# Kernel optimization log

Measured on AMD Instinct MI355X. Metric: run time of the kernel, lower is better.

## Reference

```python
import jax, jax.numpy as jnp
import numpy as np

D_STATE = 16
D_CONV = 4


def _ln_cf(x, w, b, eps=1e-6):
    # channels_first LayerNorm over dim 1 of (B,C,H,W)
    u = x.mean(1, keepdims=True)
    s = ((x - u) ** 2).mean(1, keepdims=True)
    return w[:, None, None] * ((x - u) / jnp.sqrt(s + eps)) + b[:, None, None]


def _ln_last(x, w, b, eps=1e-5):
    u = x.mean(-1, keepdims=True)
    s = ((x - u) ** 2).mean(-1, keepdims=True)
    return (x - u) / jnp.sqrt(s + eps) * w + b


def _mamba(xn, Win, convw, convb, Wx, Wdt, bdt, Alog, Dp):
    # xn: (B, L, d_model); returns (B, L, d_inner) (out_proj is Identity in this module)
    B, L, _ = xn.shape
    di = Win.shape[0] // 2
    xz = xn @ Win.T                                   # (B,L,2*di), in_proj bias=False
    xc, z = xz[..., :di], xz[..., di:]
    # causal depthwise conv1d along L (pad left d_conv-1, slice == torch pad+trim)
    xt = jnp.pad(xc.transpose(0, 2, 1), ((0, 0), (0, 0), (D_CONV - 1, 0)))
    xt = jax.lax.conv_general_dilated(xt, convw[:, None, :], (1,), 'VALID',
                                      dimension_numbers=('NCH', 'OIH', 'NCH'),
                                      feature_group_count=di)
    xs = jax.nn.silu(xt + convb[None, :, None]).transpose(0, 2, 1)  # (B,L,di)
    dtr = Wdt.shape[1]
    x_dbl = xs @ Wx.T                                 # (B,L,dtr+2*ds)
    dt = x_dbl[..., :dtr]
    Bm = x_dbl[..., dtr:dtr + D_STATE]                # (B,L,ds)
    Cm = x_dbl[..., dtr + D_STATE:]                   # (B,L,ds)
    delta = jax.nn.softplus(dt @ Wdt.T + bdt)         # (B,L,di)
    A = -jnp.exp(Alog)                                # (di,ds)
    dA = jnp.exp(delta[..., None] * A)                # (B,L,di,ds)
    dBx = delta[..., None] * Bm[:, :, None, :] * xs[..., None]

    def step(h, ab):
        a, b2 = ab
        h = a * h + b2
        return h, h

    h0 = jnp.zeros((B, di, D_STATE), xn.dtype)
    _, hs = jax.lax.scan(step, h0, (dA.transpose(1, 0, 2, 3), dBx.transpose(1, 0, 2, 3)))
    y = jnp.einsum('lbds,bls->bld', hs, Cm) + xs * Dp
    return y * jax.nn.silu(z)


def _dwconv2d(u, k, dil):
    c = k.shape[0]
    return jax.lax.conv_general_dilated(u, k[:, None], (1, 1),
                                        [(dil, dil), (dil, dil)],
                                        rhs_dilation=(dil, dil),
                                        dimension_numbers=('NCHW', 'OIHW', 'NCHW'),
                                        feature_group_count=c)


def _block(x, gamma1, gamma2, ln1_w, ln1_b, mn_w, mn_b,
           f_Win, f_convw, f_convb, f_Wx, f_Wdt, f_bdt, f_Alog, f_D,
           b_Win, b_convw, b_convb, b_Wx, b_Wdt, b_bdt, b_Alog, b_D,
           Wout, msff_win, msff_dw1, msff_dw2, msff_dw3, msff_wout):
    B, C, H, W = x.shape
    L = H * W
    # --- BiPixelMambaLayer branch ---
    x1 = _ln_cf(x, ln1_w, ln1_b)                       # norm1 (channels_first)
    xf = x1.reshape(B, C, L).transpose(0, 2, 1)        # (B,L,C)
    xn = _ln_last(xf, mn_w, mn_b)                      # inner nn.LayerNorm (eps=1e-5)
    yf = _mamba(xn, f_Win, f_convw, f_convb, f_Wx, f_Wdt, f_bdt, f_Alog, f_D)
    yb = _mamba(xn[:, ::-1], b_Win, b_convw, b_convb, b_Wx, b_Wdt, b_bdt, b_Alog, b_D)
    yo = (yf + yb[:, ::-1]) @ Wout.T                   # shared out_proj (bias=False)
    x = x + gamma1[:, None, None] * (yo.transpose(0, 2, 1).reshape(B, C, H, W) + x1)
    # --- MSFF branch (norm1 reused) ---
    inp = x
    xm = _ln_cf(x, ln1_w, ln1_b)
    h = jnp.einsum('oc,bchw->bohw', msff_win, xm)      # project_in (1x1x1 conv, depth=1)
    hid = msff_dw1.shape[0]
    h1 = _dwconv2d(h[:, :hid], msff_dw1, 1)            # Conv3d 3x3x3 w/ depth=1 == 2D center slice
    h2 = _dwconv2d(h[:, hid:2 * hid], msff_dw2, 2)
    h3 = _dwconv2d(h[:, 2 * hid:], msff_dw3, 3)
    g = jax.nn.gelu(h1, approximate=False) * h2 * h3
    xm = jnp.einsum('oc,bchw->bohw', msff_wout, g)     # project_out
    return inp + gamma2[:, None, None] * xm


def setup_inputs() -> dict:
    key = jax.random.key(0)
    ks = jax.random.split(key, 40)
    dim, di, dtr, ds, hid, Bn, H, W = 96, 192, 6, 16, 192, 2, 64, 64
    r = lambda i, shape, s=0.05: jax.random.normal(ks[i], shape, jnp.float32) * s
    inp = {
        'x': r(0, (Bn, dim, H, W), 1.0),
        'gamma1': r(1, (dim,), 0.1), 'gamma2': r(2, (dim,), 0.1),
        'ln1_w': 1.0 + r(3, (dim,), 0.1), 'ln1_b': r(4, (dim,), 0.1),
        'mn_w': 1.0 + r(5, (dim,), 0.1), 'mn_b': r(6, (dim,), 0.1),
    }
    i = 7
    for p in ('f_', 'b_'):
        inp[p + 'Win'] = r(i, (2 * di, dim)); i += 1
        inp[p + 'convw'] = r(i, (di, D_CONV), 0.2); i += 1
        inp[p + 'convb'] = r(i, (di,), 0.1); i += 1
        inp[p + 'Wx'] = r(i, (dtr + 2 * ds, di)); i += 1
        inp[p + 'Wdt'] = r(i, (di, dtr), 0.1); i += 1
        inp[p + 'bdt'] = r(i, (di,), 0.1); i += 1
        inp[p + 'Alog'] = jax.random.uniform(ks[i], (di, ds), jnp.float32, 0.0, 2.5); i += 1
        inp[p + 'D'] = r(i, (di,), 0.5); i += 1
    inp['Wout'] = r(i, (dim, di)); i += 1
    inp['msff_win'] = r(i, (3 * hid, dim)); i += 1
    inp['msff_dw1'] = r(i, (hid, 3, 3), 0.2); i += 1
    inp['msff_dw2'] = r(i, (hid, 3, 3), 0.2); i += 1
    inp['msff_dw3'] = r(i, (hid, 3, 3), 0.2); i += 1
    inp['msff_wout'] = r(i, (dim, hid)); i += 1
    return inp


def reference(x, gamma1, gamma2, ln1_w, ln1_b, mn_w, mn_b,
              f_Win, f_convw, f_convb, f_Wx, f_Wdt, f_bdt, f_Alog, f_D,
              b_Win, b_convw, b_convb, b_Wx, b_Wdt, b_bdt, b_Alog, b_D,
              Wout, msff_win, msff_dw1, msff_dw2, msff_dw3, msff_wout):
    return _block(x, gamma1, gamma2, ln1_w, ln1_b, mn_w, mn_b,
                  f_Win, f_convw, f_convb, f_Wx, f_Wdt, f_bdt, f_Alog, f_D,
                  b_Win, b_convw, b_convb, b_Wx, b_Wdt, b_bdt, b_Alog, b_D,
                  Wout, msff_win, msff_dw1, msff_dw2, msff_dw3, msff_wout)
```

## Files before the change

kernel.cpp:

```cpp
#include <hip/hip_runtime.h>
#include <hip/hip_bf16.h>
#include <math.h>

typedef __hip_bfloat16 bf16;
typedef _Float16 f16;
typedef f16  f16x8  __attribute__((ext_vector_type(8)));
typedef short short8 __attribute__((ext_vector_type(8)));
typedef unsigned short ushort8 __attribute__((ext_vector_type(8)));
typedef float floatx4 __attribute__((ext_vector_type(4)));

#define L_SEQ 4096
#define BATCH 2
#define DIM   96
#define DI    192
#define DS    16
#define HID   192
#define NPOS  (BATCH * L_SEQ)
#define NCH   256
#define CHUNK 16
#define GRP   16
#define NGRP  (NCH / GRP)
#define NREC  (2 * BATCH * DI)
#define LDBL  40
#define PLANE (4 * NCH * DI * 8)
#define LOG2E 1.44269504088896f
#define TP    32

__device__ __forceinline__ float silu_f(float x) { return x / (1.f + __expf(-x)); }
__device__ __forceinline__ float softplus_f(float x) {
    return fmaxf(x, 0.f) + __logf(1.f + __expf(-fabsf(x)));
}
__device__ __forceinline__ float b2f(bf16 v) { return __bfloat162float(v); }
__device__ __forceinline__ float us2f(unsigned short u) {
    union { unsigned int i; float f; } cv; cv.i = ((unsigned int)u) << 16; return cv.f;
}

__global__ void k_ln12_prep(const float* __restrict__ x,
                            const float* __restrict__ ln1w, const float* __restrict__ ln1b,
                            const float* __restrict__ mnw,  const float* __restrict__ mnb,
                            bf16* __restrict__ XNbf,
                            const float* __restrict__ fWin, const float* __restrict__ bWin,
                            const float* __restrict__ fWx,  const float* __restrict__ bWx,
                            const float* __restrict__ Wout, const float* __restrict__ mwin,
                            const float* __restrict__ mwout,
                            const float* __restrict__ fAlog, const float* __restrict__ bAlog,
                            const float* __restrict__ mdw1, const float* __restrict__ mdw2,
                            const float* __restrict__ mdw3,
                            bf16* __restrict__ war, float* __restrict__ a2tab,
                            float* __restrict__ mdwt) {
    __shared__ float xt[DIM][TP + 1];
    __shared__ float rs[8][TP], rss[8][TP];
    __shared__ float uu[TP], rr[TP];
    if (blockIdx.x >= NPOS / TP) {
        int i = (blockIdx.x - NPOS / TP) * 256 + threadIdx.x;
        if (i < 180480) {
            float v;
            if (i < 36864)        v = fWin[i];
            else if (i < 73728)   v = bWin[i - 36864];
            else if (i < 81024)   v = fWx[i - 73728];
            else if (i < 88320)   v = bWx[i - 81024];
            else if (i < 106752)  v = Wout[i - 88320];
            else if (i < 162048)  v = mwin[i - 106752];
            else                  v = mwout[i - 162048];
            war[i] = __float2bfloat16(v);
        } else if (i < 186624) {
            int j = i - 180480;
            int dirq = j / 3072, rem = j % 3072;
            const float* al = dirq ? bAlog : fAlog;
            a2tab[j] = -__expf(al[rem]) * LOG2E;
        } else if (i < 191808) {
            int j = i - 186624;
            int cv = j / 1728, rem = j % 1728;
            int tap = rem / 192, c = rem % 192;
            const float* src = (cv == 0) ? mdw1 : (cv == 1) ? mdw2 : mdw3;
            mdwt[j] = src[c * 9 + tap];
        }
        return;
    }
    int p0 = blockIdx.x * TP;
    int b = p0 >> 12, l0 = p0 & (L_SEQ - 1);
    int t = threadIdx.x;
    int tg = t >> 5, li = t & 31;

    for (int idx = t; idx < DIM * TP; idx += 256) {
        int c = idx >> 5, q = idx & 31;
        xt[c][q] = x[((size_t)(b * DIM + c)) * L_SEQ + l0 + q];
    }
    __syncthreads();
    {
        float s = 0.f, ss = 0.f;
        for (int c = tg; c < DIM; c += 8) { float v = xt[c][li]; s += v; ss += v * v; }
        rs[tg][li] = s; rss[tg][li] = ss;
    }
    __syncthreads();
    if (t < TP) {
        float s = 0.f, ss = 0.f;
#pragma unroll
        for (int g = 0; g < 8; g++) { s += rs[g][t]; ss += rss[g][t]; }
        float u = s / DIM;
        uu[t] = u; rr[t] = rsqrtf(ss / DIM - u * u + 1e-6f);
    }
    __syncthreads();
    {
        float u = uu[li], r = rr[li];
        float s2 = 0.f, ss2 = 0.f;
        for (int c = tg; c < DIM; c += 8) {
            float tv = ln1w[c] * (xt[c][li] - u) * r + ln1b[c];
            xt[c][li] = tv;
            s2 += tv; ss2 += tv * tv;
        }
        rs[tg][li] = s2; rss[tg][li] = ss2;
    }
    __syncthreads();
    if (t < TP) {
        float s = 0.f, ss = 0.f;
#pragma unroll
        for (int g = 0; g < 8; g++) { s += rs[g][t]; ss += rss[g][t]; }
        float u = s / DIM;
        uu[t] = u; rr[t] = rsqrtf(ss / DIM - u * u + 1e-5f);
    }
    __syncthreads();
    for (int idx = t; idx < DIM * TP; idx += 256) {
        int q = idx / DIM, c = idx % DIM;
        XNbf[(size_t)(p0 + q) * DIM + c] =
            __float2bfloat16((xt[c][q] - uu[q]) * rr[q] * mnw[c] + mnb[c]);
    }
}

__global__ void mfma_nt_dir(const bf16* __restrict__ A0, const bf16* __restrict__ A1,
                            const bf16* __restrict__ W0, const bf16* __restrict__ W1,
                            void* __restrict__ C0, void* __restrict__ C1,
                            int M, int N, int K, int ldc, int pad6, int obf) {
    int z = blockIdx.z;
    const bf16* A = z ? A1 : A0;
    const bf16* W = z ? W1 : W0;
    void* C = z ? C1 : C0;
    int wave = threadIdx.x >> 6, lane = threadIdx.x & 63;
    int m0 = blockIdx.x * 64 + wave * 16;
    int n0 = blockIdx.y * 64;
    int lm = lane & 15, quad = lane >> 4;
    const short* Ap = (const short*)A + (size_t)(m0 + lm) * K + quad * 8;
    const short* Wp = (const short*)W;
    floatx4 acc[4];
#pragma unroll
    for (int t = 0; t < 4; t++) acc[t] = (floatx4){0.f, 0.f, 0.f, 0.f};
    for (int k0 = 0; k0 < K; k0 += 32) {
        short8 a = *(const short8*)(Ap + k0);
#pragma unroll
        for (int t = 0; t < 4; t++) {
            int n = n0 + t * 16 + lm;
            short8 b = (n < N) ? *(const short8*)(Wp + (size_t)n * K + k0 + quad * 8)
                               : (short8){0,0,0,0,0,0,0,0};
            acc[t] = __builtin_amdgcn_mfma_f32_16x16x32_bf16(a, b, acc[t], 0, 0, 0);
        }
    }
#pragma unroll
    for (int t = 0; t < 4; t++) {
        int n = n0 + t * 16 + lm;
        if (n < N) {
            int nn = (pad6 && n >= 6) ? n + 2 : n;
#pragma unroll
            for (int r = 0; r < 4; r++) {
                int m = m0 + quad * 4 + r;
                if (obf) ((bf16*)C)[(size_t)m * ldc + nn] = __float2bfloat16(acc[t][r]);
                else     ((float*)C)[(size_t)m * ldc + nn] = acc[t][r];
            }
        }
    }
}

__global__ void k_conv_dbl(const bf16* __restrict__ XZF, const bf16* __restrict__ XZB,
                           const float* __restrict__ fw, const float* __restrict__ fb,
                           const float* __restrict__ bw, const float* __restrict__ bb,
                           const bf16* __restrict__ fWxB, const bf16* __restrict__ bWxB,
                           float* __restrict__ DBLF, float* __restrict__ DBLB,
                           bf16* __restrict__ XSF, bf16* __restrict__ XSB) {
    __shared__ __align__(16) unsigned short xs_t[64][200];
    int dirb = blockIdx.y;
    int p0 = blockIdx.x * 64;
    const bf16* XZ = dirb ? XZB : XZF;
    const float* cw = dirb ? bw : fw;
    const float* cb = dirb ? bb : fb;
    bf16* XS = dirb ? XSB : XSF;

    for (int u = threadIdx.x; u < 64 * 24; u += 256) {
        int dg = u % 24, pl = u / 24;
        int p = p0 + pl;
        int b = p >> 12, l = p & (L_SEQ - 1);
        int d0 = dg * 8;
        float4 w[8];
#pragma unroll
        for (int j = 0; j < 8; j++) w[j] = *(const float4*)(cw + (d0 + j) * 4);
        float acc[8];
#pragma unroll
        for (int j = 0; j < 8; j++) acc[j] = cb[d0 + j];
#pragma unroll
        for (int k = 0; k < 4; k++) {
            int ls = dirb ? (l + 3 - k) : (l - 3 + k);
            if (ls >= 0 && ls < L_SEQ) {
                ushort8 xv = *(const ushort8*)((const unsigned short*)XZ +
                               ((size_t)(b * L_SEQ + ls)) * 384 + d0);
#pragma unroll
                for (int j = 0; j < 8; j++) {
                    float wk = (k == 0) ? w[j].x : (k == 1) ? w[j].y : (k == 2) ? w[j].z : w[j].w;
                    acc[j] += wk * us2f(xv[j]);
                }
            }
        }
        ushort8 ov;
#pragma unroll
        for (int j = 0; j < 8; j++) {
            bf16 tv = __float2bfloat16(silu_f(acc[j]));
            ov[j] = *(unsigned short*)&tv;
        }
        *(ushort8*)((unsigned short*)XS + (size_t)p * DI + d0) = ov;
        *(ushort8*)&xs_t[pl][d0] = ov;
    }
    __syncthreads();
    int t = threadIdx.x;
    int w = t >> 6, lane = t & 63;
    int lm = lane & 15, quad = lane >> 4;
    const bf16* Wx = dirb ? bWxB : fWxB;
    float* DBL = dirb ? DBLB : DBLF;
    floatx4 acc[3];
#pragma unroll
    for (int tt = 0; tt < 3; tt++) acc[tt] = (floatx4){0.f, 0.f, 0.f, 0.f};
    const unsigned short* ar = &xs_t[w * 16 + lm][0];
#pragma unroll
    for (int k = 0; k < 6; k++) {
        int k0 = k * 32 + quad * 8;
        short8 a = *(const short8*)(ar + k0);
#pragma unroll
        for (int tt = 0; tt < 3; tt++) {
            int n = tt * 16 + lm;
            short8 bq = (n < 38) ? *(const short8*)((const short*)Wx + n * 192 + k0)
                                 : (short8){0,0,0,0,0,0,0,0};
            acc[tt] = __builtin_amdgcn_mfma_f32_16x16x32_bf16(a, bq, acc[tt], 0, 0, 0);
        }
    }
#pragma unroll
    for (int tt = 0; tt < 3; tt++) {
        int n = tt * 16 + lm;
        if (n < 38) {
            int nn = (n >= 6) ? n + 2 : n;
#pragma unroll
            for (int r = 0; r < 4; r++) {
                int m = p0 + w * 16 + quad * 4 + r;
                DBL[(size_t)m * LDBL + nn] = acc[tt][r];
            }
        }
    }
}

__global__ void k_scan_p1g(const float* __restrict__ DBLF, const float* __restrict__ DBLB,
                           const bf16* __restrict__ XSF,  const bf16* __restrict__ XSB,
                           const float* __restrict__ fWdt, const float* __restrict__ fbdt,
                           const float* __restrict__ bWdt, const float* __restrict__ bbdt,
                           const float* __restrict__ a2tab,
                           f16* __restrict__ Pexc, f16* __restrict__ Qexc,
                           float* __restrict__ Pg, float* __restrict__ Qg) {
    __shared__ f16x8 Pl[2][GRP][16];
    __shared__ f16x8 Ql[2][GRP][16];
    int dsl = blockIdx.x, grp = blockIdx.y, dirb = blockIdx.z;
    int t = threadIdx.x;
    int chunk = t >> 4, dl = t & 15;
    int d = dsl * 16 + dl;
    int b = dirb & 1, dir = dirb >> 1;
    int gc = grp * GRP + chunk;

    const float* DBL = dir ? DBLB : DBLF;
    const bf16*  XS  = dir ? XSB  : XSF;
    const float* wdt = (dir ? bWdt : fWdt) + d * 6;
    float bdtv = (dir ? bbdt : fbdt)[d];

    float wd[6];
#pragma unroll
    for (int r = 0; r < 6; r++) wd[r] = wdt[r];
    const float* a2p = a2tab + (dir * DI + d) * 16;
    float A2[16], h[16];
#pragma unroll
    for (int v = 0; v < 4; v++) {
        float4 a2v = *(const float4*)(a2p + 4 * v);
        A2[4*v] = a2v.x; A2[4*v+1] = a2v.y; A2[4*v+2] = a2v.z; A2[4*v+3] = a2v.w;
    }
#pragma unroll
    for (int s = 0; s < 16; s++) h[s] = 0.f;

    int l = dir ? (L_SEQ - 1 - gc * CHUNK) : gc * CHUNK;
    int stp = dir ? -1 : 1;
    float sumdel = 0.f;

    for (int i = 0; i < CHUNK; i++) {
        size_t p = (size_t)b * L_SEQ + l;
        const float* row = DBL + p * LDBL;
        float dtv = bdtv;
#pragma unroll
        for (int r = 0; r < 6; r++) dtv += row[r] * wd[r];
        float del = softplus_f(dtv);
        float xs  = b2f(XS[p * DI + d]);
        const float4* bm = (const float4*)(row + 8);
        float4 B0 = bm[0], B1 = bm[1], B2 = bm[2], B3 = bm[3];
        float Bm[16] = {B0.x,B0.y,B0.z,B0.w, B1.x,B1.y,B1.z,B1.w,
                        B2.x,B2.y,B2.z,B2.w, B3.x,B3.y,B3.z,B3.w};
        float dx = del * xs;
        sumdel += del;
#pragma unroll
        for (int s = 0; s < 16; s++) {
            float dA = exp2f(del * A2[s]);
            h[s] = dA * h[s] + dx * Bm[s];
        }
        l += stp;
    }
    {
        f16x8 p0, p1, q0, q1;
#pragma unroll
        for (int j = 0; j < 8; j++) {
            q0[j] = (f16)h[j];
            q1[j] = (f16)h[8 + j];
            p0[j] = (f16)exp2f(A2[j] * sumdel);
            p1[j] = (f16)exp2f(A2[8 + j] * sumdel);
        }
        Pl[0][chunk][dl] = p0; Pl[1][chunk][dl] = p1;
        Ql[0][chunk][dl] = q0; Ql[1][chunk][dl] = q1;
    }
    __syncthreads();

    {
        int s  = t & 15, dl2 = t >> 4;
        int s8 = s >> 3, sl = s & 7;
        f16* Pp = (f16*)&Pl[s8][0][dl2];
        f16* Qp = (f16*)&Ql[s8][0][dl2];
        float runP = 1.f, runQ = 0.f;
#pragma unroll
        for (int c = 0; c < GRP; c++) {
            float pv = (float)Pp[c * 128 + sl];
            float qv = (float)Qp[c * 128 + sl];
            Pp[c * 128 + sl] = (f16)runP;
            Qp[c * 128 + sl] = (f16)runQ;
            runQ = pv * runQ + qv;
            runP *= pv;
        }
        int d2 = dsl * 16 + dl2;
        size_t gidx = (((size_t)(dirb * NGRP + grp)) * DI + d2) * 16 + s;
        Pg[gidx] = runP;
        Qg[gidx] = runQ;
    }
    __syncthreads();

    {
        size_t base = ((size_t)(dirb * NCH + gc) * DI + d) * 8;
        *(f16x8*)(Pexc + base)         = Pl[0][chunk][dl];
        *(f16x8*)(Pexc + PLANE + base) = Pl[1][chunk][dl];
        *(f16x8*)(Qexc + base)         = Ql[0][chunk][dl];
        *(f16x8*)(Qexc + PLANE + base) = Ql[1][chunk][dl];
    }
}

__global__ void k_scan_p3g(const float* __restrict__ DBLF, const float* __restrict__ DBLB,
                           const bf16* __restrict__ XSF,  const bf16* __restrict__ XSB,
                           const bf16* __restrict__ XZF,  const bf16* __restrict__ XZB,
                           const float* __restrict__ fWdt, const float* __restrict__ fbdt,
                           const float* __restrict__ bWdt, const float* __restrict__ bbdt,
                           const float* __restrict__ a2tab,
                           const float* __restrict__ fD,    const float* __restrict__ bD,
                           const f16* __restrict__ Pexc, const f16* __restrict__ Qexc,
                           const float* __restrict__ Pg, const float* __restrict__ Qg,
                           bf16* __restrict__ YSF, bf16* __restrict__ YSB) {
    __shared__ float qx[16][17];
    int dsl = blockIdx.x, grp = blockIdx.y, dirb = blockIdx.z;
    int t = threadIdx.x;
    {
        int dl = t >> 4, s = t & 15;
        int d2 = dsl * 16 + dl;
        float runQ = 0.f;
        for (int g = 0; g < grp; g++) {
            size_t i = (((size_t)(dirb * NGRP + g)) * DI + d2) * 16 + s;
            runQ = Pg[i] * runQ + Qg[i];
        }
        qx[dl][s] = runQ;
    }
    __syncthreads();

    int chunk = t >> 4, dl = t & 15;
    int d = dsl * 16 + dl;
    int gc = grp * GRP + chunk;
    int b = dirb & 1, dir = dirb >> 1;

    const float* DBL = dir ? DBLB : DBLF;
    const bf16*  XS  = dir ? XSB  : XSF;
    const bf16*  XZ  = dir ? XZB  : XZF;
    const float* wdt = (dir ? bWdt : fWdt) + d * 6;
    float bdtv = (dir ? bbdt : fbdt)[d];
    float Dp = dir ? bD[d] : fD[d];
    bf16* Y = dir ? YSB : YSF;

    float wd[6];
#pragma unroll
    for (int r = 0; r < 6; r++) wd[r] = wdt[r];
    const float* a2p = a2tab + (dir * DI + d) * 16;
    float A2[16], h[16];
#pragma unroll
    for (int v = 0; v < 4; v++) {
        float4 a2v = *(const float4*)(a2p + 4 * v);
        A2[4*v] = a2v.x; A2[4*v+1] = a2v.y; A2[4*v+2] = a2v.z; A2[4*v+3] = a2v.w;
    }
    {
        size_t base = ((size_t)(dirb * NCH + gc) * DI + d) * 8;
        f16x8 pe0 = *(const f16x8*)(Pexc + base);
        f16x8 pe1 = *(const f16x8*)(Pexc + PLANE + base);
        f16x8 qe0 = *(const f16x8*)(Qexc + base);
        f16x8 qe1 = *(const f16x8*)(Qexc + PLANE + base);
#pragma unroll
        for (int j = 0; j < 8; j++) {
            h[j]     = (float)pe0[j] * qx[dl][j]     + (float)qe0[j];
            h[8 + j] = (float)pe1[j] * qx[dl][8 + j] + (float)qe1[j];
        }
    }

    int l = dir ? (L_SEQ - 1 - gc * CHUNK) : gc * CHUNK;
    int stp = dir ? -1 : 1;

    for (int i = 0; i < CHUNK; i++) {
        size_t p = (size_t)b * L_SEQ + l;
        const float* row = DBL + p * LDBL;
        float dtv = bdtv;
#pragma unroll
        for (int r = 0; r < 6; r++) dtv += row[r] * wd[r];
        float del = softplus_f(dtv);
        float xs  = b2f(XS[p * DI + d]);
        float z   = b2f(XZ[p * 384 + 192 + d]);
        const float4* bm = (const float4*)(row + 8);
        float4 B0 = bm[0], B1 = bm[1], B2 = bm[2], B3 = bm[3];
        float4 C0 = bm[4], C1 = bm[5], C2 = bm[6], C3 = bm[7];
        float Bm[16] = {B0.x,B0.y,B0.z,B0.w, B1.x,B1.y,B1.z,B1.w,
                        B2.x,B2.y,B2.z,B2.w, B3.x,B3.y,B3.z,B3.w};
        float Cm[16] = {C0.x,C0.y,C0.z,C0.w, C1.x,C1.y,C1.z,C1.w,
                        C2.x,C2.y,C2.z,C2.w, C3.x,C3.y,C3.z,C3.w};
        float dx = del * xs;
        float pr = 0.f;
#pragma unroll
        for (int s = 0; s < 16; s++) {
            float dA = exp2f(del * A2[s]);
            h[s] = dA * h[s] + dx * Bm[s];
            pr += h[s] * Cm[s];
        }
        Y[p * DI + d] = __float2bfloat16((pr + xs * Dp) * silu_f(z));
        l += stp;
    }
}

__global__ void k_out_mid(const bf16* __restrict__ Y1, const bf16* __restrict__ Y2,
                          const bf16* __restrict__ W,
                          const float* __restrict__ x, const float* __restrict__ gamma1,
                          const float* __restrict__ ln1w, const float* __restrict__ ln1b,
                          float* __restrict__ XMID, bf16* __restrict__ XM2cl) {
    __shared__ float yt[DIM][TP + 1];
    __shared__ float xt[DIM][TP + 1];
    __shared__ float rs[8][TP], rss[8][TP];
    __shared__ float uu[TP], rr[TP];
    int p0 = blockIdx.x * TP;
    int b = p0 >> 12, l0 = p0 & (L_SEQ - 1);
    int t = threadIdx.x;
    int tg = t >> 5, li = t & 31;

    {
        int w = t >> 6, lane = t & 63;
        int lm = lane & 15, quad = lane >> 4;
        int mh = w & 1, nb = (w >> 1) * 3;
        const short* A1p = (const short*)Y1 + (size_t)(p0 + mh * 16 + lm) * 192 + quad * 8;
        const short* A2p = (const short*)Y2 + (size_t)(p0 + mh * 16 + lm) * 192 + quad * 8;
        const short* Wp  = (const short*)W;
        floatx4 acc[3];
#pragma unroll
        for (int tt = 0; tt < 3; tt++) acc[tt] = (floatx4){0.f, 0.f, 0.f, 0.f};
#pragma unroll
        for (int k = 0; k < 6; k++) {
            int k0 = k * 32;
            short8 a1 = *(const short8*)(A1p + k0);
            short8 a2 = *(const short8*)(A2p + k0);
#pragma unroll
            for (int tt = 0; tt < 3; tt++) {
                int n = (nb + tt) * 16 + lm;
                short8 bq = *(const short8*)(Wp + (size_t)n * 192 + k0 + quad * 8);
                acc[tt] = __builtin_amdgcn_mfma_f32_16x16x32_bf16(a1, bq, acc[tt], 0, 0, 0);
                acc[tt] = __builtin_amdgcn_mfma_f32_16x16x32_bf16(a2, bq, acc[tt], 0, 0, 0);
            }
        }
#pragma unroll
        for (int tt = 0; tt < 3; tt++) {
            int c = (nb + tt) * 16 + lm;
#pragma unroll
            for (int r = 0; r < 4; r++)
                yt[c][mh * 16 + quad * 4 + r] = acc[tt][r];
        }
    }
    for (int idx = t; idx < DIM * TP; idx += 256) {
        int c = idx >> 5, q = idx & 31;
        xt[c][q] = x[((size_t)(b * DIM + c)) * L_SEQ + l0 + q];
    }
    __syncthreads();
    {
        float s = 0.f, ss = 0.f;
        for (int c = tg; c < DIM; c += 8) { float v = xt[c][li]; s += v; ss += v * v; }
        rs[tg][li] = s; rss[tg][li] = ss;
    }
    __syncthreads();
    if (t < TP) {
        float s = 0.f, ss = 0.f;
#pragma unroll
        for (int g = 0; g < 8; g++) { s += rs[g][t]; ss += rss[g][t]; }
        float u = s / DIM;
        uu[t] = u; rr[t] = rsqrtf(ss / DIM - u * u + 1e-6f);
    }
    __syncthreads();
    {
        float u = uu[li], r = rr[li];
        float s = 0.f, ss = 0.f;
        for (int c = tg; c < DIM; c += 8) {
            float xv = xt[c][li];
            float x1 = ln1w[c] * (xv - u) * r + ln1b[c];
            float v = xv + gamma1[c] * (yt[c][li] + x1);
            XMID[((size_t)(b * DIM + c)) * L_SEQ + l0 + li] = v;
            xt[c][li] = v;
            s += v; ss += v * v;
        }
        rs[tg][li] = s; rss[tg][li] = ss;
    }
    __syncthreads();
    if (t < TP) {
        float s = 0.f, ss = 0.f;
#pragma unroll
        for (int g = 0; g < 8; g++) { s += rs[g][t]; ss += rss[g][t]; }
        float u = s / DIM;
        uu[t] = u; rr[t] = rsqrtf(ss / DIM - u * u + 1e-6f);
    }
    __syncthreads();
    for (int idx = t; idx < DIM * TP; idx += 256) {
        int q = idx / DIM, c = idx % DIM;
        XM2cl[(size_t)(p0 + q) * DIM + c] =
            __float2bfloat16(ln1w[c] * (xt[c][q] - uu[q]) * rr[q] + ln1b[c]);
    }
}

__global__ void mfma_nt(const bf16* __restrict__ A, const bf16* __restrict__ W,
                        bf16* __restrict__ C, int M, int N, int K, int ldc) {
    int wave = threadIdx.x >> 6, lane = threadIdx.x & 63;
    int m0 = blockIdx.x * 64 + wave * 16;
    int n0 = blockIdx.y * 64;
    int lm = lane & 15, quad = lane >> 4;
    const short* Ap = (const short*)A + (size_t)(m0 + lm) * K + quad * 8;
    const short* Wp = (const short*)W;
    floatx4 acc[4];
#pragma unroll
    for (int t = 0; t < 4; t++) acc[t] = (floatx4){0.f, 0.f, 0.f, 0.f};
    for (int k0 = 0; k0 < K; k0 += 32) {
        short8 a = *(const short8*)(Ap + k0);
#pragma unroll
        for (int t = 0; t < 4; t++) {
            int n = n0 + t * 16 + lm;
            short8 b = (n < N) ? *(const short8*)(Wp + (size_t)n * K + k0 + quad * 8)
                               : (short8){0,0,0,0,0,0,0,0};
            acc[t] = __builtin_amdgcn_mfma_f32_16x16x32_bf16(a, b, acc[t], 0, 0, 0);
        }
    }
#pragma unroll
    for (int t = 0; t < 4; t++) {
        int n = n0 + t * 16 + lm;
        if (n < N) {
#pragma unroll
            for (int r = 0; r < 4; r++) {
                int m = m0 + quad * 4 + r;
                C[(size_t)m * ldc + n] = __float2bfloat16(acc[t][r]);
            }
        }
    }
}

__global__ void k_msff_outres(const bf16* __restrict__ H, const float* __restrict__ mdwt,
                              const bf16* __restrict__ mwoutB,
                              const float* __restrict__ XMID, const float* __restrict__ gamma2,
                              float* __restrict__ out) {
    __shared__ __align__(16) unsigned short gt[32][200];
    int p0 = blockIdx.x * 32;
    int t = threadIdx.x;
    const unsigned short* Hu = (const unsigned short*)H;

    for (int u = t; u < 32 * 24; u += 256) {
        int cg = u % 24, pl = u / 24;
        int p = p0 + pl;
        int c0 = cg * 8;
        int b = p >> 12, l = p & (L_SEQ - 1);
        int y = l >> 6, xc = l & 63;
        float a1[8] = {}, a2[8] = {}, a3[8] = {};
#pragma unroll
        for (int ky = 0; ky < 3; ky++) {
#pragma unroll
            for (int kx = 0; kx < 3; kx++) {
                int tap = ky * 3 + kx;
                {
                    int y1 = y + (ky - 1), x1 = xc + (kx - 1);
                    if (y1 >= 0 && y1 < 64 && x1 >= 0 && x1 < 64) {
                        float4 w0 = *(const float4*)(mdwt + tap * 192 + c0);
                        float4 w1 = *(const float4*)(mdwt + tap * 192 + c0 + 4);
                        ushort8 hv = *(const ushort8*)(Hu +
                            ((size_t)(b * L_SEQ + y1 * 64 + x1)) * 576 + c0);
                        float wv[8] = {w0.x,w0.y,w0.z,w0.w, w1.x,w1.y,w1.z,w1.w};
#pragma unroll
                        for (int j = 0; j < 8; j++) a1[j] += wv[j] * us2f(hv[j]);
                    }
                }
                {
                    int y2 = y + (ky - 1) * 2, x2 = xc + (kx - 1) * 2;
                    if (y2 >= 0 && y2 < 64 && x2 >= 0 && x2 < 64) {
                        float4 w0 = *(const float4*)(mdwt + (9 + tap) * 192 + c0);
                        float4 w1 = *(const float4*)(mdwt + (9 + tap) * 192 + c0 + 4);
                        ushort8 hv = *(const ushort8*)(Hu +
                            ((size_t)(b * L_SEQ + y2 * 64 + x2)) * 576 + 192 + c0);
                        float wv[8] = {w0.x,w0.y,w0.z,w0.w, w1.x,w1.y,w1.z,w1.w};
#pragma unroll
                        for (int j = 0; j < 8; j++) a2[j] += wv[j] * us2f(hv[j]);
                    }
                }
                {
                    int y3 = y + (ky - 1) * 3, x3 = xc + (kx - 1) * 3;
                    if (y3 >= 0 && y3 < 64 && x3 >= 0 && x3 < 64) {
                        float4 w0 = *(const float4*)(mdwt + (18 + tap) * 192 + c0);
                        float4 w1 = *(const float4*)(mdwt + (18 + tap) * 192 + c0 + 4);
                        ushort8 hv = *(const ushort8*)(Hu +
                            ((size_t)(b * L_SEQ + y3 * 64 + x3)) * 576 + 384 + c0);
                        float wv[8] = {w0.x,w0.y,w0.z,w0.w, w1.x,w1.y,w1.z,w1.w};
#pragma unroll
                        for (int j = 0; j < 8; j++) a3[j] += wv[j] * us2f(hv[j]);
                    }
                }
            }
        }
        ushort8 ov;
#pragma unroll
        for (int j = 0; j < 8; j++) {
            float ge = 0.5f * a1[j] * (1.f + erff(a1[j] * 0.70710678118f));
            bf16 tv = __float2bfloat16(ge * a2[j] * a3[j]);
            ov[j] = *(unsigned short*)&tv;
        }
        *(ushort8*)&gt[pl][c0] = ov;
    }
    __syncthreads();
    int w = t >> 6, lane = t & 63;
    int lm = lane & 15, quad = lane >> 4;
    int nt = w & 1, mb = (w >> 1) * 3;
    floatx4 acc[3];
#pragma unroll
    for (int tt = 0; tt < 3; tt++) acc[tt] = (floatx4){0.f, 0.f, 0.f, 0.f};
    const unsigned short* br = &gt[nt * 16 + lm][0];
#pragma unroll
    for (int k = 0; k < 6; k++) {
        int k0 = k * 32 + quad * 8;
        short8 bq = *(const short8*)(br + k0);
#pragma unroll
        for (int tt = 0; tt < 3; tt++) {
            int m = (mb + tt) * 16 + lm;
            short8 a = *(const short8*)((const short*)mwoutB + m * 192 + k0);
            acc[tt] = __builtin_amdgcn_mfma_f32_16x16x32_bf16(a, bq, acc[tt], 0, 0, 0);
        }
    }
    int b = p0 >> 12, l0 = p0 & (L_SEQ - 1);
#pragma unroll
    for (int tt = 0; tt < 3; tt++) {
#pragma unroll
        for (int r = 0; r < 4; r++) {
            int m = (mb + tt) * 16 + quad * 4 + r;
            size_t idx = ((size_t)(b * DIM + m)) * L_SEQ + l0 + nt * 16 + lm;
            out[idx] = XMID[idx] + gamma2[m] * acc[tt][r];
        }
    }
}

extern "C" void kernel_launch(void* const* d_in, const int* in_sizes, int n_in,
                              void* d_out, int out_size, void* d_ws, size_t ws_size,
                              hipStream_t stream) {
    const float* x      = (const float*)d_in[0];
    const float* gamma1 = (const float*)d_in[1];
    const float* gamma2 = (const float*)d_in[2];
    const float* ln1w   = (const float*)d_in[3];
    const float* ln1b   = (const float*)d_in[4];
    const float* mnw    = (const float*)d_in[5];
    const float* mnb    = (const float*)d_in[6];
    const float* fWin   = (const float*)d_in[7];
    const float* fconvw = (const float*)d_in[8];
    const float* fconvb = (const float*)d_in[9];
    const float* fWx    = (const float*)d_in[10];
    const float* fWdt   = (const float*)d_in[11];
    const float* fbdt   = (const float*)d_in[12];
    const float* fAlog  = (const float*)d_in[13];
    const float* fD     = (const float*)d_in[14];
    const float* bWin   = (const float*)d_in[15];
    const float* bconvw = (const float*)d_in[16];
    const float* bconvb = (const float*)d_in[17];
    const float* bWx    = (const float*)d_in[18];
    const float* bWdt   = (const float*)d_in[19];
    const float* bbdt   = (const float*)d_in[20];
    const float* bAlog  = (const float*)d_in[21];
    const float* bD     = (const float*)d_in[22];
    const float* Wout   = (const float*)d_in[23];
    const float* mwin   = (const float*)d_in[24];
    const float* mdw1   = (const float*)d_in[25];
    const float* mdw2   = (const float*)d_in[26];
    const float* mdw3   = (const float*)d_in[27];
    const float* mwout  = (const float*)d_in[28];
    float* out = (float*)d_out;

    float* ws = (float*)d_ws;
    bf16*  XNbf  = (bf16*)(ws);
    bf16*  XZF   = (bf16*)(ws + 393216);
    bf16*  XZB   = (bf16*)(ws + 1966080);
    bf16*  XSF   = (bf16*)(ws + 3538944);
    bf16*  XSB   = (bf16*)(ws + 4325376);
    float* DBLF  = ws + 5111808;
    float* DBLB  = ws + 5439488;
    f16*   Ph    = (f16*)(ws + 5767168);
    f16*   Qh    = (f16*)(ws + 8912896);
    bf16*  YSFbf = (bf16*)(ws + 12058624);
    bf16*  YSBbf = (bf16*)(ws + 12845056);
    float* XMID  = ws + 14417920;
    bf16*  XM2cl = (bf16*)(ws + 15204352);
    bf16*  Hcl   = (bf16*)(ws + 15597568);
    bf16*  WAR   = (bf16*)(ws + 18743296);
    float* A2tab = ws + 18833536;
    float* MDWT  = ws + 18839680;
    float* Pgb   = ws + 18844864;
    float* Qgb   = ws + 19041472;

    const bf16* fWinB  = WAR;
    const bf16* bWinB  = WAR + 36864;
    const bf16* fWxB   = WAR + 73728;
    const bf16* bWxB   = WAR + 81024;
    const bf16* WoutB  = WAR + 88320;
    const bf16* mwinB  = WAR + 106752;
    const bf16* mwoutB = WAR + 162048;

    k_ln12_prep<<<NPOS / TP + 750, 256, 0, stream>>>(
        x, ln1w, ln1b, mnw, mnb, XNbf,
        fWin, bWin, fWx, bWx, Wout, mwin, mwout,
        fAlog, bAlog, mdw1, mdw2, mdw3, WAR, A2tab, MDWT);
    mfma_nt_dir<<<dim3(128, 6, 2), 256, 0, stream>>>(XNbf, XNbf, fWinB, bWinB,
                                                     XZF, XZB, NPOS, 384, DIM, 384, 0, 1);
    k_conv_dbl<<<dim3(NPOS / 64, 2), 256, 0, stream>>>(
        XZF, XZB, fconvw, fconvb, bconvw, bconvb,
        fWxB, bWxB, DBLF, DBLB, XSF, XSB);
    k_scan_p1g<<<dim3(DI / 16, NGRP, 4), 256, 0, stream>>>(
        DBLF, DBLB, XSF, XSB, fWdt, fbdt, bWdt, bbdt,
        A2tab, Ph, Qh, Pgb, Qgb);
    k_scan_p3g<<<dim3(DI / 16, NGRP, 4), 256, 0, stream>>>(
        DBLF, DBLB, XSF, XSB, XZF, XZB,
        fWdt, fbdt, bWdt, bbdt, A2tab, fD, bD,
        Ph, Qh, Pgb, Qgb, YSFbf, YSBbf);
    k_out_mid<<<NPOS / TP, 256, 0, stream>>>(
        YSFbf, YSBbf, WoutB, x, gamma1, ln1w, ln1b, XMID, XM2cl);
    mfma_nt<<<dim3(128, 9), 256, 0, stream>>>(XM2cl, mwinB, Hcl, NPOS, 576, DIM, 576);
    k_msff_outres<<<NPOS / 32, 256, 0, stream>>>(Hcl, MDWT, mwoutB, XMID, gamma2, out);
}
```

Baseline: 269.1 us.

## Fuse MSFF input projection GEMM into out_mid kernel via LDS-staged LayerNorm output

```diff
diff --git a/kernel.cpp b/kernel.cpp
--- a/kernel.cpp
+++ b/kernel.cpp
@@ -453,11 +453,13 @@
                           const bf16* __restrict__ W,
                           const float* __restrict__ x, const float* __restrict__ gamma1,
                           const float* __restrict__ ln1w, const float* __restrict__ ln1b,
-                          float* __restrict__ XMID, bf16* __restrict__ XM2cl) {
+                          const bf16* __restrict__ mwinB,
+                          float* __restrict__ XMID, bf16* __restrict__ H) {
     __shared__ float yt[DIM][TP + 1];
     __shared__ float xt[DIM][TP + 1];
     __shared__ float rs[8][TP], rss[8][TP];
     __shared__ float uu[TP], rr[TP];
+    __shared__ __align__(16) unsigned short xmt[TP][104];
     int p0 = blockIdx.x * TP;
     int b = p0 >> 12, l0 = p0 & (L_SEQ - 1);
     int t = threadIdx.x;
@@ -537,40 +539,33 @@
     __syncthreads();
     for (int idx = t; idx < DIM * TP; idx += 256) {
         int q = idx / DIM, c = idx % DIM;
-        XM2cl[(size_t)(p0 + q) * DIM + c] =
-            __float2bfloat16(ln1w[c] * (xt[c][q] - uu[q]) * rr[q] + ln1b[c]);
-    }
-}
-
-__global__ void mfma_nt(const bf16* __restrict__ A, const bf16* __restrict__ W,
-                        bf16* __restrict__ C, int M, int N, int K, int ldc) {
-    int wave = threadIdx.x >> 6, lane = threadIdx.x & 63;
-    int m0 = blockIdx.x * 64 + wave * 16;
-    int n0 = blockIdx.y * 64;
-    int lm = lane & 15, quad = lane >> 4;
-    const short* Ap = (const short*)A + (size_t)(m0 + lm) * K + quad * 8;
-    const short* Wp = (const short*)W;
-    floatx4 acc[4];
-#pragma unroll
-    for (int t = 0; t < 4; t++) acc[t] = (floatx4){0.f, 0.f, 0.f, 0.f};
-    for (int k0 = 0; k0 < K; k0 += 32) {
-        short8 a = *(const short8*)(Ap + k0);
-#pragma unroll
-        for (int t = 0; t < 4; t++) {
-            int n = n0 + t * 16 + lm;
-            short8 b = (n < N) ? *(const short8*)(Wp + (size_t)n * K + k0 + quad * 8)
-                               : (short8){0,0,0,0,0,0,0,0};
-            acc[t] = __builtin_amdgcn_mfma_f32_16x16x32_bf16(a, b, acc[t], 0, 0, 0);
-        }
-    }
-#pragma unroll
-    for (int t = 0; t < 4; t++) {
-        int n = n0 + t * 16 + lm;
-        if (n < N) {
+        bf16 tv = __float2bfloat16(ln1w[c] * (xt[c][q] - uu[q]) * rr[q] + ln1b[c]);
+        xmt[q][c] = *(unsigned short*)&tv;
+    }
+    __syncthreads();
+    {
+        int w = t >> 6, lane = t & 63;
+        int lm = lane & 15, quad = lane >> 4;
+        int mh = w & 1, ng = w >> 1;
+        const unsigned short* ar = &xmt[mh * 16 + lm][0];
+        short8 a[3];
+#pragma unroll
+        for (int k = 0; k < 3; k++)
+            a[k] = *(const short8*)(ar + k * 32 + quad * 8);
+        const short* Wp = (const short*)mwinB;
+#pragma unroll
+        for (int tt = 0; tt < 18; tt++) {
+            int n = (ng * 18 + tt) * 16 + lm;
+            floatx4 acc = (floatx4){0.f, 0.f, 0.f, 0.f};
+#pragma unroll
+            for (int k = 0; k < 3; k++) {
+                short8 bq = *(const short8*)(Wp + (size_t)n * 96 + k * 32 + quad * 8);
+                acc = __builtin_amdgcn_mfma_f32_16x16x32_bf16(a[k], bq, acc, 0, 0, 0);
+            }
 #pragma unroll
             for (int r = 0; r < 4; r++) {
-                int m = m0 + quad * 4 + r;
-                C[(size_t)m * ldc + n] = __float2bfloat16(acc[t][r]);
+                int m = p0 + mh * 16 + quad * 4 + r;
+                H[(size_t)m * 576 + n] = __float2bfloat16(acc[r]);
             }
         }
     }
@@ -722,7 +717,6 @@
     bf16*  YSFbf = (bf16*)(ws + 12058624);
     bf16*  YSBbf = (bf16*)(ws + 12845056);
     float* XMID  = ws + 14417920;
-    bf16*  XM2cl = (bf16*)(ws + 15204352);
     bf16*  Hcl   = (bf16*)(ws + 15597568);
     bf16*  WAR   = (bf16*)(ws + 18743296);
     float* A2tab = ws + 18833536;
@@ -755,7 +749,6 @@
         fWdt, fbdt, bWdt, bbdt, A2tab, fD, bD,
         Ph, Qh, Pgb, Qgb, YSFbf, YSBbf);
     k_out_mid<<<NPOS / TP, 256, 0, stream>>>(
-        YSFbf, YSBbf, WoutB, x, gamma1, ln1w, ln1b, XMID, XM2cl);
-    mfma_nt<<<dim3(128, 9), 256, 0, stream>>>(XM2cl, mwinB, Hcl, NPOS, 576, DIM, 576);
+        YSFbf, YSBbf, WoutB, x, gamma1, ln1w, ln1b, mwinB, XMID, Hcl);
     k_msff_outres<<<NPOS / 32, 256, 0, stream>>>(Hcl, MDWT, mwoutB, XMID, gamma2, out);
 }
```

After: 264.5 us. Within noise of the previous version (-1.7%).
